# Optimization experiments

Hardware: AMD Instinct MI355X
Metric: run time of the kernel (lower is better)

Reference implementation:

```python
import jax, jax.numpy as jnp
import numpy as np

B, T, D, H, L = 128, 512, 512, 512, 2

def setup_inputs() -> dict:
    key = jax.random.key(0)
    k1, k2 = jax.random.split(key)
    x = jax.random.normal(k1, (B, T, D), dtype=jnp.float32)
    hiddens = jnp.zeros((L, 2, B, H), dtype=jnp.float32)  # [layer, (h,c), batch, hidden]
    # stacked per-layer fused-gate weights; torch Linear(in+hid, 4*hid)
    W = jax.random.normal(k2, (L, D + H, 4 * H), dtype=jnp.float32) * (1.0 / np.sqrt(D + H))
    b = jnp.zeros((L, 4 * H), dtype=jnp.float32)
    return {"x": x, "hiddens": hiddens, "W": W, "b": b}

def reference(x, hiddens, W, b):
    num_layers = W.shape[0]

    def step(hid, x_t):
        inp = x_t
        new = []
        for l in range(num_layers):
            h, c = hid[l, 0], hid[l, 1]
            gates = jnp.concatenate([inp, h], axis=-1) @ W[l] + b[l]  # [B, 4H]
            i, f, g, o = jnp.split(gates, 4, axis=-1)
            i = jax.nn.sigmoid(i)
            f = jax.nn.sigmoid(f)
            g = jnp.tanh(g)
            o = jax.nn.sigmoid(o)
            c_t = f * c + i * g
            h_t = o * jnp.tanh(c_t)
            new.append(jnp.stack([h_t, c_t], axis=0))
            inp = h_t
        hid = jnp.stack(new, axis=0)
        return hid, inp  # emit top-layer h per timestep

    hiddens_final, outs = jax.lax.scan(step, hiddens, jnp.swapaxes(x, 0, 1))
    outputs = jnp.swapaxes(outs, 0, 1)  # [B, T, H]
    return outputs, hiddens_final
```

## Files before the change

### kernel.cpp

```cpp
#include <hip/hip_runtime.h>
#include <stdint.h>

typedef __attribute__((ext_vector_type(4))) int   i32x4;
typedef __attribute__((ext_vector_type(8))) short bf16x8;
typedef __attribute__((ext_vector_type(4))) float f32x4;

#define DEV static __device__ __forceinline__

constexpr int  kB = 128, kT = 512, kD = 512, kH = 512;
constexpr int  kGC = 2048;
constexpr int  ROWS = 32;
constexpr int  NG = 4;
constexpr int  NJ = 32;
constexpr int  NTHREADS = 512;
constexpr size_t SLOT_ELEMS = (size_t)kB * kH;
constexpr size_t WIMG_ELEMS = (size_t)2 * NJ * 4 * 32 * 512;
constexpr size_t WIMG_BYTES = WIMG_ELEMS * 2;
constexpr int  RFULL = kT + 1;
constexpr int  FLAG_STRIDE = 128;
constexpr size_t FLAG_TOTAL = (size_t)2 * NG * kT * FLAG_STRIDE;

DEV ushort f2bf(float f) {
  uint32_t u = __float_as_uint(f);
  u += 0x7fff + ((u >> 16) & 1);
  return (ushort)(u >> 16);
}
DEV int pk2(float a, float b) { return (int)((uint32_t)f2bf(a) | ((uint32_t)f2bf(b) << 16)); }
DEV float sigf(float v)  { return 1.f / (1.f + __expf(-v)); }
DEV float tanhf_(float v){ return 1.f - 2.f / (__expf(2.f * v) + 1.f); }

DEV uint64_t ald64(const uint64_t* p) {
  return __hip_atomic_load(p, __ATOMIC_RELAXED, __HIP_MEMORY_SCOPE_AGENT);
}

DEV void poll32(const uint8_t* fb) {
  const uint64_t* p = reinterpret_cast<const uint64_t*>(fb);
  constexpr uint64_t ONE = 0x0101010101010101ull;
  for (;;) {
    uint64_t a = ald64(p) & ald64(p + 1) & ald64(p + 2) & ald64(p + 3);
    if (a == ONE) return;
    __builtin_amdgcn_s_sleep(1);
  }
}

__global__ void prep_w(const float* __restrict__ W, ushort* __restrict__ wimg) {
  uint32_t idx = blockIdx.x * 256u + threadIdx.x;
  int e = idx & 7, lane = (idx >> 3) & 63, ks = (idx >> 9) & 31;
  int G = (idx >> 14) & 3, j = (idx >> 16) & 31, l = (idx >> 21) & 1;
  int k = ks * 32 + ((lane >> 4) << 3) + e;
  int c = G * 512 + j * 16 + (lane & 15);
  wimg[idx] = f2bf(W[(size_t)l * 1024 * 2048 + (size_t)k * 2048 + c]);
}

__global__ void prep_init(const float* __restrict__ hiddens, ushort* __restrict__ r0, ushort* __restrict__ r1) {
  uint32_t idx = blockIdx.x * 256u + threadIdx.x;
  int l = idx >> 16; uint32_t r = idx & 65535u;
  ushort v = f2bf(hiddens[(size_t)(l * 2 + 0) * 65536 + r]);
  (l ? r1 : r0)[r] = v;
}

DEV void stage_h(ushort* Ab, const ushort* rbase, int g, int tid) {
  #pragma unroll
  for (int p = 0; p < 4; ++p) {
    int o = (tid + p * NTHREADS) * 16, row = o >> 10, kb = o & 1023;
    i32x4 v = *reinterpret_cast<const i32x4*>(rbase + (size_t)(g * ROWS + row) * kH + (kb >> 1));
    *reinterpret_cast<i32x4*>(reinterpret_cast<char*>(Ab) + ((row * 1024 + kb) ^ ((row & 7) << 4))) = v;
  }
}

__launch_bounds__(NTHREADS, 2)
__global__ void lstm_v3(const float* __restrict__ x, const float* __restrict__ hiddens,
                        const float* __restrict__ bias, const ushort* __restrict__ wimg,
                        ushort* __restrict__ ring0, ushort* __restrict__ ring1,
                        uint8_t* __restrict__ flags, float* __restrict__ out) {
  __shared__ ushort AbufX[ROWS * 512];
  __shared__ ushort AbufH[ROWS * 512];
  __shared__ float  gbuf[4][ROWS][17];

  const int tid  = threadIdx.x;
  const int lane = tid & 63;
  const int wv   = tid >> 6;
  const int G    = wv & 3;
  const int rf   = wv >> 2;
  const int j    = blockIdx.x & 31;
  const int g    = (blockIdx.x >> 5) & 3;
  const int l    = blockIdx.x >> 7;

  __threadfence();

  i32x4 wr[32];
  {
    const ushort* base = wimg + (((size_t)(l * NJ + j) * 4 + G) * 32) * 512 + lane * 8;
    #pragma unroll
    for (int ks = 0; ks < 32; ++ks)
      wr[ks] = *reinterpret_cast<const i32x4*>(base + ks * 512);
  }
  const float bval = bias[l * kGC + G * 512 + j * 16 + (lane & 15)];
  const int urow = tid >> 4, ucol = tid & 15;
  float creg = hiddens[((size_t)(l * 2 + 1) * kB + (g * ROWS + urow)) * kH + j * 16 + ucol];

  ushort* rrec = l ? ring1 : ring0;
  uint8_t* myflags = flags + (size_t)(l * NG + g) * kT * FLAG_STRIDE;
  const uint8_t* xflags = flags + (size_t)g * kT * FLAG_STRIDE;

  const int arow  = rf * 16 + (lane & 15);
  const int koff  = (lane >> 4) << 3;
  const int abase = arow * 1024;
  const int aswz  = (arow & 7) << 4;

  for (int t = 0; t < kT; ++t) {
    if (l == 1) {
      poll32(xflags + (size_t)t * FLAG_STRIDE);
      stage_h(AbufX, ring0 + (size_t)(t + 1) * SLOT_ELEMS, g, tid);
    } else {
      #pragma unroll
      for (int p = 0; p < 4; ++p) {
        int o = (tid + p * NTHREADS) * 16, row = o >> 10, kb = o & 1023;
        const float* src = x + ((size_t)(g * ROWS + row) * kT + t) * kD + (kb >> 1);
        f32x4 f0 = *reinterpret_cast<const f32x4*>(src);
        f32x4 f1 = *reinterpret_cast<const f32x4*>(src + 4);
        i32x4 v;
        v[0] = pk2(f0[0], f0[1]); v[1] = pk2(f0[2], f0[3]);
        v[2] = pk2(f1[0], f1[1]); v[3] = pk2(f1[2], f1[3]);
        *reinterpret_cast<i32x4*>(reinterpret_cast<char*>(AbufX) + ((row * 1024 + kb) ^ ((row & 7) << 4))) = v;
      }
    }
    __syncthreads();

    f32x4 acc = {};
    #pragma unroll
    for (int ks = 0; ks < 16; ++ks) {
      int off = (abase + ((ks * 32 + koff) << 1)) ^ aswz;
      i32x4 av = *reinterpret_cast<const i32x4*>(reinterpret_cast<const char*>(AbufX) + off);
      acc = __builtin_amdgcn_mfma_f32_16x16x32_bf16(
              *reinterpret_cast<bf16x8*>(&av), *reinterpret_cast<bf16x8*>(&wr[ks]), acc, 0, 0, 0);
    }

    if (t > 0) poll32(myflags + (size_t)(t - 1) * FLAG_STRIDE);
    stage_h(AbufH, rrec + (size_t)t * SLOT_ELEMS, g, tid);
    __syncthreads();

    #pragma unroll
    for (int ks = 0; ks < 16; ++ks) {
      int off = (abase + ((ks * 32 + koff) << 1)) ^ aswz;
      i32x4 av = *reinterpret_cast<const i32x4*>(reinterpret_cast<const char*>(AbufH) + off);
      acc = __builtin_amdgcn_mfma_f32_16x16x32_bf16(
              *reinterpret_cast<bf16x8*>(&av), *reinterpret_cast<bf16x8*>(&wr[16 + ks]), acc, 0, 0, 0);
    }

    #pragma unroll
    for (int q = 0; q < 4; ++q) {
      float v2 = acc[q] + bval;
      v2 = (G == 2) ? tanhf_(v2) : sigf(v2);
      gbuf[G][rf * 16 + ((lane >> 4) << 2) + q][lane & 15] = v2;
    }
    __syncthreads();

    float hh;
    {
      float iv = gbuf[0][urow][ucol], fv = gbuf[1][urow][ucol];
      float gv = gbuf[2][urow][ucol], ov = gbuf[3][urow][ucol];
      creg = fv * creg + iv * gv;
      hh = ov * tanhf_(creg);
      uint32_t me    = f2bf(hh);
      uint32_t other = (uint32_t)__shfl_xor((int)me, 1);
      if (!(ucol & 1)) {
        uint32_t pkv = me | (other << 16);
        uint32_t* dst = (uint32_t*)(rrec + (size_t)(t + 1) * SLOT_ELEMS
                                    + (size_t)(g * ROWS + urow) * kH + j * 16 + ucol);
        __hip_atomic_store(dst, pkv, __ATOMIC_RELAXED, __HIP_MEMORY_SCOPE_AGENT);
      }
    }
    asm volatile("s_waitcnt vmcnt(0)" ::: "memory");
    __syncthreads();
    if (tid == 0)
      __hip_atomic_store(myflags + (size_t)t * FLAG_STRIDE + j, (uint8_t)1,
                         __ATOMIC_RELAXED, __HIP_MEMORY_SCOPE_AGENT);

    {
      int b = g * ROWS + urow;
      if (l == 1) out[((size_t)b * kT + t) * kH + j * 16 + ucol] = hh;
      if (t == kT - 1) {
        size_t hb = (size_t)kB * kT * kH;
        out[hb + ((size_t)(l * 2 + 0) * kB + b) * kH + j * 16 + ucol] = hh;
        out[hb + ((size_t)(l * 2 + 1) * kB + b) * kH + j * 16 + ucol] = creg;
      }
    }
  }
}


template<bool BIG>
DEV void stage_ring(ushort* Abuf_, const ushort* rbase, int g, int tid) {
  #pragma unroll
  for (int p = 0; p < 4; ++p) {
    int o = (tid + p * NTHREADS) * 16;
    int row = o >> 10, kb = o & 1023;
    const ushort* src = rbase + (size_t)(g * ROWS + row) * kH + (kb >> 1);
    i32x4 v;
    if (BIG) {
      v = *reinterpret_cast<const i32x4*>(src);
    } else {
      uint64_t lo = __hip_atomic_load((const uint64_t*)src,       __ATOMIC_RELAXED, __HIP_MEMORY_SCOPE_AGENT);
      uint64_t hi = __hip_atomic_load((const uint64_t*)(src + 4), __ATOMIC_RELAXED, __HIP_MEMORY_SCOPE_AGENT);
      v[0] = (int)(uint32_t)lo; v[1] = (int)(uint32_t)(lo >> 32);
      v[2] = (int)(uint32_t)hi; v[3] = (int)(uint32_t)(hi >> 32);
    }
    *reinterpret_cast<i32x4*>(reinterpret_cast<char*>(Abuf_) + ((row * 1024 + kb) ^ ((row & 7) << 4))) = v;
  }
}

template<bool BIG>
__launch_bounds__(NTHREADS, 2)
__global__ void lstm_main(const float* __restrict__ x, const float* __restrict__ hiddens,
                          const float* __restrict__ bias, const ushort* __restrict__ wimg,
                          ushort* __restrict__ ring0, ushort* __restrict__ ring1,
                          int* __restrict__ cnt, int* __restrict__ cons0,
                          float* __restrict__ out, int R0, int R1) {
  __shared__ ushort Abuf[ROWS * 512];
  __shared__ float  gbuf[4][ROWS][16];
  __shared__ float  cbuf[ROWS][16];
  __shared__ float  hbuf[ROWS][16];

  const int tid  = threadIdx.x;
  const int lane = tid & 63;
  const int wv   = tid >> 6;
  const int G    = wv & 3;
  const int rf   = wv >> 2;
  const int j    = blockIdx.x & 31;
  const int g    = (blockIdx.x >> 5) & 3;
  const int l    = blockIdx.x >> 7;

  __threadfence();

  i32x4 wr[32];
  {
    const ushort* base = wimg + (((size_t)(l * NJ + j) * 4 + G) * 32) * 512 + lane * 8;
    #pragma unroll
    for (int ks = 0; ks < 32; ++ks)
      wr[ks] = *reinterpret_cast<const i32x4*>(base + ks * 512);
  }
  const float bval = bias[l * kGC + G * 512 + j * 16 + (lane & 15)];
  {
    int row = tid >> 4, col = tid & 15;
    cbuf[row][col] = hiddens[((size_t)(l * 2 + 1) * kB + (g * ROWS + row)) * kH + j * 16 + col];
  }
  int* mycnt = cnt + (l * NG + g) * kT;
  int* c0cnt = cnt + g * kT;
  ushort* rrec = l ? ring1 : ring0;
  const int Rrec = l ? R1 : R0;

  const int arow  = rf * 16 + (lane & 15);
  const int koff  = (lane >> 4) << 3;
  const int abase = arow * 1024;
  const int aswz  = (arow & 7) << 4;

  __syncthreads();

  for (int t = 0; t < kT; ++t) {
    if (l == 1) {
      if (tid == 0) {
        while (__hip_atomic_load(&c0cnt[t], __ATOMIC_RELAXED, __HIP_MEMORY_SCOPE_AGENT) < NJ)
          __builtin_amdgcn_s_sleep(2);
      }
      __syncthreads();
      stage_ring<BIG>(Abuf, ring0 + (size_t)((t + 1) % R0) * SLOT_ELEMS, g, tid);
    } else {
      #pragma unroll
      for (int p = 0; p < 4; ++p) {
        int o = (tid + p * NTHREADS) * 16;
        int row = o >> 10, kb = o & 1023;
        const float* src = x + ((size_t)(g * ROWS + row) * kT + t) * kD + (kb >> 1);
        f32x4 f0 = *reinterpret_cast<const f32x4*>(src);
        f32x4 f1 = *reinterpret_cast<const f32x4*>(src + 4);
        i32x4 v;
        v[0] = pk2(f0[0], f0[1]); v[1] = pk2(f0[2], f0[3]);
        v[2] = pk2(f1[0], f1[1]); v[3] = pk2(f1[2], f1[3]);
        *reinterpret_cast<i32x4*>(reinterpret_cast<char*>(Abuf) + ((row * 1024 + kb) ^ ((row & 7) << 4))) = v;
      }
    }
    __syncthreads();
    if (!BIG && l == 1 && tid == 0)
      __hip_atomic_fetch_add(&cons0[g * kT + t], 1, __ATOMIC_RELAXED, __HIP_MEMORY_SCOPE_AGENT);

    f32x4 acc = {};
    #pragma unroll
    for (int ks = 0; ks < 16; ++ks) {
      int off = (abase + ((ks * 32 + koff) << 1)) ^ aswz;
      i32x4 av = *reinterpret_cast<const i32x4*>(reinterpret_cast<const char*>(Abuf) + off);
      acc = __builtin_amdgcn_mfma_f32_16x16x32_bf16(
              *reinterpret_cast<bf16x8*>(&av), *reinterpret_cast<bf16x8*>(&wr[ks]), acc, 0, 0, 0);
    }
    __syncthreads();

    if (t > 0) {
      if (tid == 0) {
        while (__hip_atomic_load(&mycnt[t - 1], __ATOMIC_RELAXED, __HIP_MEMORY_SCOPE_AGENT) < NJ)
          __builtin_amdgcn_s_sleep(2);
        if (!BIG && l == 0 && t >= R0) {
          while (__hip_atomic_load(&cons0[g * kT + (t - R0)], __ATOMIC_RELAXED, __HIP_MEMORY_SCOPE_AGENT) < NJ)
            __builtin_amdgcn_s_sleep(2);
        }
      }
      __syncthreads();
    }
    stage_ring<BIG>(Abuf, rrec + (size_t)(t % Rrec) * SLOT_ELEMS, g, tid);
    __syncthreads();

    #pragma unroll
    for (int ks = 0; ks < 16; ++ks) {
      int off = (abase + ((ks * 32 + koff) << 1)) ^ aswz;
      i32x4 av = *reinterpret_cast<const i32x4*>(reinterpret_cast<const char*>(Abuf) + off);
      acc = __builtin_amdgcn_mfma_f32_16x16x32_bf16(
              *reinterpret_cast<bf16x8*>(&av), *reinterpret_cast<bf16x8*>(&wr[16 + ks]), acc, 0, 0, 0);
    }

    #pragma unroll
    for (int q = 0; q < 4; ++q) {
      float v2 = acc[q] + bval;
      v2 = (G == 2) ? tanhf_(v2) : sigf(v2);
      gbuf[G][rf * 16 + ((lane >> 4) << 2) + q][lane & 15] = v2;
    }
    __syncthreads();

    {
      int row = tid >> 4, col = tid & 15;
      float iv = gbuf[0][row][col], fv = gbuf[1][row][col];
      float gv = gbuf[2][row][col], ov = gbuf[3][row][col];
      float cc = fv * cbuf[row][col] + iv * gv;
      cbuf[row][col] = cc;
      float hh = ov * tanhf_(cc);
      hbuf[row][col] = hh;
      int b = g * ROWS + row;
      if (l == 1) out[((size_t)b * kT + t) * kH + j * 16 + col] = hh;
      if (t == kT - 1) {
        size_t hb = (size_t)kB * kT * kH;
        out[hb + ((size_t)(l * 2 + 0) * kB + b) * kH + j * 16 + col] = hh;
        out[hb + ((size_t)(l * 2 + 1) * kB + b) * kH + j * 16 + col] = cc;
      }
    }
    __syncthreads();

    if (tid < 256) {
      int row = tid >> 3, cp = tid & 7;
      uint32_t pkv = (uint32_t)f2bf(hbuf[row][2 * cp]) | ((uint32_t)f2bf(hbuf[row][2 * cp + 1]) << 16);
      uint32_t* dst = (uint32_t*)(rrec + (size_t)((t + 1) % Rrec) * SLOT_ELEMS
                                  + (size_t)(g * ROWS + row) * kH + j * 16 + 2 * cp);
      __hip_atomic_store(dst, pkv, __ATOMIC_RELAXED, __HIP_MEMORY_SCOPE_AGENT);
    }
    asm volatile("s_waitcnt vmcnt(0)" ::: "memory");
    __syncthreads();
    if (tid == 0)
      __hip_atomic_fetch_add(&mycnt[t], 1, __ATOMIC_RELAXED, __HIP_MEMORY_SCOPE_AGENT);
  }
}

extern "C" void kernel_launch(void* const* d_in, const int* in_sizes, int n_in,
                              void* d_out, int out_size, void* d_ws, size_t ws_size,
                              hipStream_t stream) {
  const float* x  = (const float*)d_in[0];
  const float* hd = (const float*)d_in[1];
  const float* W  = (const float*)d_in[2];
  const float* b  = (const float*)d_in[3];
  float* out = (float*)d_out;

  char* ws = (char*)d_ws;
  ushort* wimg = (ushort*)ws;
  uint8_t* flags = (uint8_t*)(ws + WIMG_BYTES);
  int* cnt  = (int*)(ws + WIMG_BYTES + FLAG_TOTAL);
  int* cons = (int*)(ws + WIMG_BYTES + FLAG_TOTAL + 16384);
  size_t ringoff = WIMG_BYTES + FLAG_TOTAL + 32768;
  size_t avail = ws_size > ringoff ? ws_size - ringoff : 0;
  long rmax = (long)(avail / (2 * SLOT_ELEMS * 2));
  int R = (rmax >= RFULL) ? RFULL : (rmax >= 16 ? 16 : (rmax >= 2 ? (int)rmax : 2));
  ushort* ring0 = (ushort*)(ws + ringoff);
  ushort* ring1 = ring0 + (size_t)R * SLOT_ELEMS;

  prep_w<<<(int)(WIMG_ELEMS / 256), 256, 0, stream>>>(W, wimg);
  prep_init<<<(2 * kB * kH) / 256, 256, 0, stream>>>(hd, ring0, ring1);
  if (R == RFULL) {
    hipMemsetAsync(flags, 0, FLAG_TOTAL, stream);
    lstm_v3<<<256, NTHREADS, 0, stream>>>(x, hd, b, wimg, ring0, ring1, flags, out);
  } else {
    hipMemsetAsync(ws + WIMG_BYTES + FLAG_TOTAL, 0, 32768, stream);
    lstm_main<false><<<256, NTHREADS, 0, stream>>>(x, hd, b, wimg, ring0, ring1, cnt, cons, out, R, R);
  }
}
```

Measured before the change: 2.145 ms.

## Split waves by K-half so input GEMM overlaps recurrent-state staging and prefetch x

The eight waves are reassigned so half compute the input-projection MFMAs (two gates each) while the other half poll the recurrence flag and stage the previous hidden state into LDS, then compute the recurrent-half MFMAs. Partial sums from both halves go to a doubled gate buffer and are summed with bias before the activations in the elementwise update. Layer 0 also prefetches the next timestep's x into registers so global load latency is hidden behind the current step. This aims to shorten the serial critical path per timestep, at the cost of more LDS traffic, extra registers for the prefetch and an extra reduction.

```diff
diff --git a/kernel.cpp b/kernel.cpp
--- a/kernel.cpp
+++ b/kernel.cpp
@@ -68,35 +68,52 @@
   }
 }
 
+DEV void stage_h256(ushort* Ab, const ushort* rbase, int g, int tid256) {
+  #pragma unroll
+  for (int p = 0; p < 8; ++p) {
+    int o = (tid256 + p * 256) * 16, row = o >> 10, kb = o & 1023;
+    i32x4 v = *reinterpret_cast<const i32x4*>(rbase + (size_t)(g * ROWS + row) * kH + (kb >> 1));
+    *reinterpret_cast<i32x4*>(reinterpret_cast<char*>(Ab) + ((row * 1024 + kb) ^ ((row & 7) << 4))) = v;
+  }
+}
+
 __launch_bounds__(NTHREADS, 2)
-__global__ void lstm_v3(const float* __restrict__ x, const float* __restrict__ hiddens,
+__global__ void lstm_v4(const float* __restrict__ x, const float* __restrict__ hiddens,
                         const float* __restrict__ bias, const ushort* __restrict__ wimg,
                         ushort* __restrict__ ring0, ushort* __restrict__ ring1,
                         uint8_t* __restrict__ flags, float* __restrict__ out) {
   __shared__ ushort AbufX[ROWS * 512];
   __shared__ ushort AbufH[ROWS * 512];
-  __shared__ float  gbuf[4][ROWS][17];
+  __shared__ float  gbuf[2][4][ROWS][17];
 
   const int tid  = threadIdx.x;
   const int lane = tid & 63;
   const int wv   = tid >> 6;
-  const int G    = wv & 3;
-  const int rf   = wv >> 2;
+  const int kh   = wv >> 2;
+  const int Gp   = (wv >> 1) & 1;
+  const int rf   = wv & 1;
   const int j    = blockIdx.x & 31;
   const int g    = (blockIdx.x >> 5) & 3;
   const int l    = blockIdx.x >> 7;
 
   __threadfence();
 
-  i32x4 wr[32];
+  i32x4 wrA[16], wrB[16];
   {
-    const ushort* base = wimg + (((size_t)(l * NJ + j) * 4 + G) * 32) * 512 + lane * 8;
-    #pragma unroll
-    for (int ks = 0; ks < 32; ++ks)
-      wr[ks] = *reinterpret_cast<const i32x4*>(base + ks * 512);
-  }
-  const float bval = bias[l * kGC + G * 512 + j * 16 + (lane & 15)];
+    const int GA = 2 * Gp, GB = 2 * Gp + 1;
+    const ushort* baseA = wimg + (((size_t)(l * NJ + j) * 4 + GA) * 32 + kh * 16) * 512 + lane * 8;
+    const ushort* baseB = wimg + (((size_t)(l * NJ + j) * 4 + GB) * 32 + kh * 16) * 512 + lane * 8;
+    #pragma unroll
+    for (int ks = 0; ks < 16; ++ks) {
+      wrA[ks] = *reinterpret_cast<const i32x4*>(baseA + ks * 512);
+      wrB[ks] = *reinterpret_cast<const i32x4*>(baseB + ks * 512);
+    }
+  }
   const int urow = tid >> 4, ucol = tid & 15;
+  const float b0 = bias[l * kGC + 0 * 512 + j * 16 + ucol];
+  const float b1 = bias[l * kGC + 1 * 512 + j * 16 + ucol];
+  const float b2 = bias[l * kGC + 2 * 512 + j * 16 + ucol];
+  const float b3 = bias[l * kGC + 3 * 512 + j * 16 + ucol];
   float creg = hiddens[((size_t)(l * 2 + 1) * kB + (g * ROWS + urow)) * kH + j * 16 + ucol];
 
   ushort* rrec = l ? ring1 : ring0;
@@ -108,58 +125,92 @@
   const int abase = arow * 1024;
   const int aswz  = (arow & 7) << 4;
 
+  f32x4 xr[8];
+  if (l == 0) {
+    #pragma unroll
+    for (int p = 0; p < 4; ++p) {
+      int o = (tid + p * NTHREADS) * 16, row = o >> 10, kb = o & 1023;
+      const float* src = x + ((size_t)(g * ROWS + row) * kT + 0) * kD + (kb >> 1);
+      xr[2 * p]     = *reinterpret_cast<const f32x4*>(src);
+      xr[2 * p + 1] = *reinterpret_cast<const f32x4*>(src + 4);
+    }
+  }
+
   for (int t = 0; t < kT; ++t) {
-    if (l == 1) {
+    if (l == 0) {
+      #pragma unroll
+      for (int p = 0; p < 4; ++p) {
+        int o = (tid + p * NTHREADS) * 16, row = o >> 10, kb = o & 1023;
+        i32x4 v;
+        v[0] = pk2(xr[2 * p][0], xr[2 * p][1]);  v[1] = pk2(xr[2 * p][2], xr[2 * p][3]);
+        v[2] = pk2(xr[2 * p + 1][0], xr[2 * p + 1][1]); v[3] = pk2(xr[2 * p + 1][2], xr[2 * p + 1][3]);
+        *reinterpret_cast<i32x4*>(reinterpret_cast<char*>(AbufX) + ((row * 1024 + kb) ^ ((row & 7) << 4))) = v;
+      }
+    } else {
       poll32(xflags + (size_t)t * FLAG_STRIDE);
       stage_h(AbufX, ring0 + (size_t)(t + 1) * SLOT_ELEMS, g, tid);
+    }
+    __syncthreads();
+
+    if (kh == 0) {
+      f32x4 accA = {}, accB = {};
+      #pragma unroll
+      for (int ks = 0; ks < 16; ++ks) {
+        int off = (abase + ((ks * 32 + koff) << 1)) ^ aswz;
+        i32x4 av = *reinterpret_cast<const i32x4*>(reinterpret_cast<const char*>(AbufX) + off);
+        accA = __builtin_amdgcn_mfma_f32_16x16x32_bf16(
+                 *reinterpret_cast<bf16x8*>(&av), *reinterpret_cast<bf16x8*>(&wrA[ks]), accA, 0, 0, 0);
+        accB = __builtin_amdgcn_mfma_f32_16x16x32_bf16(
+                 *reinterpret_cast<bf16x8*>(&av), *reinterpret_cast<bf16x8*>(&wrB[ks]), accB, 0, 0, 0);
+      }
+      #pragma unroll
+      for (int q = 0; q < 4; ++q) {
+        int r = rf * 16 + ((lane >> 4) << 2) + q, c = lane & 15;
+        gbuf[0][2 * Gp][r][c]     = accA[q];
+        gbuf[0][2 * Gp + 1][r][c] = accB[q];
+      }
     } else {
+      if (t > 0) poll32(myflags + (size_t)(t - 1) * FLAG_STRIDE);
+      stage_h256(AbufH, rrec + (size_t)t * SLOT_ELEMS, g, tid - 256);
+    }
+    __syncthreads();
+
+    if (l == 0 && t + 1 < kT) {
       #pragma unroll
       for (int p = 0; p < 4; ++p) {
         int o = (tid + p * NTHREADS) * 16, row = o >> 10, kb = o & 1023;
-        const float* src = x + ((size_t)(g * ROWS + row) * kT + t) * kD + (kb >> 1);
-        f32x4 f0 = *reinterpret_cast<const f32x4*>(src);
-        f32x4 f1 = *reinterpret_cast<const f32x4*>(src + 4);
-        i32x4 v;
-        v[0] = pk2(f0[0], f0[1]); v[1] = pk2(f0[2], f0[3]);
-        v[2] = pk2(f1[0], f1[1]); v[3] = pk2(f1[2], f1[3]);
-        *reinterpret_cast<i32x4*>(reinterpret_cast<char*>(AbufX) + ((row * 1024 + kb) ^ ((row & 7) << 4))) = v;
-      }
-    }
-    __syncthreads();
-
-    f32x4 acc = {};
-    #pragma unroll
-    for (int ks = 0; ks < 16; ++ks) {
-      int off = (abase + ((ks * 32 + koff) << 1)) ^ aswz;
-      i32x4 av = *reinterpret_cast<const i32x4*>(reinterpret_cast<const char*>(AbufX) + off);
-      acc = __builtin_amdgcn_mfma_f32_16x16x32_bf16(
-              *reinterpret_cast<bf16x8*>(&av), *reinterpret_cast<bf16x8*>(&wr[ks]), acc, 0, 0, 0);
-    }
-
-    if (t > 0) poll32(myflags + (size_t)(t - 1) * FLAG_STRIDE);
-    stage_h(AbufH, rrec + (size_t)t * SLOT_ELEMS, g, tid);
-    __syncthreads();
-
-    #pragma unroll
-    for (int ks = 0; ks < 16; ++ks) {
-      int off = (abase + ((ks * 32 + koff) << 1)) ^ aswz;
-      i32x4 av = *reinterpret_cast<const i32x4*>(reinterpret_cast<const char*>(AbufH) + off);
-      acc = __builtin_amdgcn_mfma_f32_16x16x32_bf16(
-              *reinterpret_cast<bf16x8*>(&av), *reinterpret_cast<bf16x8*>(&wr[16 + ks]), acc, 0, 0, 0);
-    }
-
-    #pragma unroll
-    for (int q = 0; q < 4; ++q) {
-      float v2 = acc[q] + bval;
-      v2 = (G == 2) ? tanhf_(v2) : sigf(v2);
-      gbuf[G][rf * 16 + ((lane >> 4) << 2) + q][lane & 15] = v2;
+        const float* src = x + ((size_t)(g * ROWS + row) * kT + (t + 1)) * kD + (kb >> 1);
+        xr[2 * p]     = *reinterpret_cast<const f32x4*>(src);
+        xr[2 * p + 1] = *reinterpret_cast<const f32x4*>(src + 4);
+      }
+    }
+
+    if (kh == 1) {
+      f32x4 accA = {}, accB = {};
+      #pragma unroll
+      for (int ks = 0; ks < 16; ++ks) {
+        int off = (abase + ((ks * 32 + koff) << 1)) ^ aswz;
+        i32x4 av = *reinterpret_cast<const i32x4*>(reinterpret_cast<const char*>(AbufH) + off);
+        accA = __builtin_amdgcn_mfma_f32_16x16x32_bf16(
+                 *reinterpret_cast<bf16x8*>(&av), *reinterpret_cast<bf16x8*>(&wrA[ks]), accA, 0, 0, 0);
+        accB = __builtin_amdgcn_mfma_f32_16x16x32_bf16(
+                 *reinterpret_cast<bf16x8*>(&av), *reinterpret_cast<bf16x8*>(&wrB[ks]), accB, 0, 0, 0);
+      }
+      #pragma unroll
+      for (int q = 0; q < 4; ++q) {
+        int r = rf * 16 + ((lane >> 4) << 2) + q, c = lane & 15;
+        gbuf[1][2 * Gp][r][c]     = accA[q];
+        gbuf[1][2 * Gp + 1][r][c] = accB[q];
+      }
     }
     __syncthreads();
 
     float hh;
     {
-      float iv = gbuf[0][urow][ucol], fv = gbuf[1][urow][ucol];
-      float gv = gbuf[2][urow][ucol], ov = gbuf[3][urow][ucol];
+      float iv = sigf  (gbuf[0][0][urow][ucol] + gbuf[1][0][urow][ucol] + b0);
+      float fv = sigf  (gbuf[0][1][urow][ucol] + gbuf[1][1][urow][ucol] + b1);
+      float gv = tanhf_(gbuf[0][2][urow][ucol] + gbuf[1][2][urow][ucol] + b2);
+      float ov = sigf  (gbuf[0][3][urow][ucol] + gbuf[1][3][urow][ucol] + b3);
       creg = fv * creg + iv * gv;
       hh = ov * tanhf_(creg);
       uint32_t me    = f2bf(hh);
@@ -380,7 +431,7 @@
   prep_init<<<(2 * kB * kH) / 256, 256, 0, stream>>>(hd, ring0, ring1);
   if (R == RFULL) {
     hipMemsetAsync(flags, 0, FLAG_TOTAL, stream);
-    lstm_v3<<<256, NTHREADS, 0, stream>>>(x, hd, b, wimg, ring0, ring1, flags, out);
+    lstm_v4<<<256, NTHREADS, 0, stream>>>(x, hd, b, wimg, ring0, ring1, flags, out);
   } else {
     hipMemsetAsync(ws + WIMG_BYTES + FLAG_TOTAL, 0, 32768, stream);
     lstm_main<false><<<256, NTHREADS, 0, stream>>>(x, hd, b, wimg, ring0, ring1, cnt, cons, out, R, R);
```

Measured after the change: 2.708 ms. 1.26x slower.
